# Kernel optimization log

Measured on AMD Instinct MI355X. Metric: run time of the kernel, lower is better.

Reference implementation:

```python
import jax, jax.numpy as jnp
import numpy as np

N_NODES = 100000
N_EDGES = 3200000
IN_DIM, HID1, HID2 = 128, 32, 16


def setup_inputs() -> dict:
    key = jax.random.key(0)
    ks = jax.random.split(key, 4)
    x = jax.random.normal(ks[0], (N_NODES, IN_DIM), dtype=jnp.float32)
    # glorot-ish scaling for weights
    W1 = jax.random.normal(ks[1], (IN_DIM, HID1), dtype=jnp.float32) * (1.0 / np.sqrt(IN_DIM))
    b1 = jnp.zeros((HID1,), dtype=jnp.float32)
    W2 = jax.random.normal(ks[2], (HID1, HID2), dtype=jnp.float32) * (1.0 / np.sqrt(HID1))
    b2 = jnp.zeros((HID2,), dtype=jnp.float32)
    edge_index = jax.random.randint(ks[3], (2, N_EDGES), 0, N_NODES, dtype=jnp.int64)
    return {"x": x, "W1": W1, "b1": b1, "W2": W2, "b2": b2, "edge_index": edge_index}


def _gcn_norm(edge_index, n_nodes):
    # add self loops, then symmetric normalization D^-1/2 (A+I) D^-1/2
    loops = jnp.arange(n_nodes, dtype=edge_index.dtype)
    src = jnp.concatenate([edge_index[0], loops])  # [E+N]
    dst = jnp.concatenate([edge_index[1], loops])
    deg = jax.ops.segment_sum(jnp.ones_like(dst, dtype=jnp.float32), dst, num_segments=n_nodes)
    inv_sqrt = jnp.where(deg > 0, jax.lax.rsqrt(jnp.maximum(deg, 1.0)), 0.0)
    norm = inv_sqrt[src] * inv_sqrt[dst]  # [E+N]
    return src, dst, norm


def _gcn_conv(x, W, b, src, dst, norm, n_nodes):
    xw = x @ W                                   # [N, out] transform first (out < in)
    msg = xw[src] * norm[:, None]                # gather + scale  [E+N, out]
    agg = jax.ops.segment_sum(msg, dst, num_segments=n_nodes)  # scatter-add
    return agg + b


def reference(x, W1, b1, W2, b2, edge_index):
    n = x.shape[0]
    src, dst, norm = _gcn_norm(edge_index, n)  # cached=True: same norm both layers
    h = _gcn_conv(x, W1, b1, src, dst, norm, n)
    h = jax.nn.relu(h)
    out = _gcn_conv(h, W2, b2, src, dst, norm, n)
    return out
```

## Files before the change

kernel.cpp:

```cpp
#include <hip/hip_runtime.h>
#include <hip/hip_fp16.h>


#define IN_DIM 128
#define HID1 32
#define HID2 16

#define BSHIFT 8
#define MAXNB 1024
#define SLABCAP 9216
#define P2_TILE 4096
#define P2_PER_THREAD 16

__device__ __forceinline__ void load_edge(const int* __restrict__ e32, int is64,
                                          long e, long E, int& s, int& d) {
    if (is64) { s = e32[2 * e];  d = e32[2 * E + 2 * e]; }
    else      { s = e32[e];      d = e32[E + e]; }
}

__device__ __forceinline__ void h8acc(float4& acc, uint2 u) {
    __half2 a = *(__half2*)&u.x, b = *(__half2*)&u.y;
    float2 fa = __half22float2(a), fb = __half22float2(b);
    acc.x += fa.x; acc.y += fa.y; acc.z += fb.x; acc.w += fb.y;
}

__global__ void init_cursors(const int* __restrict__ e32, int* __restrict__ flag,
                             int* __restrict__ total,
                             int* __restrict__ bucketCursor, int NB) {
    int i = blockIdx.x * blockDim.x + threadIdx.x;
    if (i < NB) bucketCursor[i] = i * SLABCAP;
    if (blockIdx.x == 0 && threadIdx.x == 0) {
        *total = 0;
        int is64 = 1;
        for (int k = 0; k < 64; ++k)
            if (e32[2 * k + 1] != 0) { is64 = 0; break; }
        *flag = is64;
    }
}

__global__ __launch_bounds__(256) void partition_edges(const int* __restrict__ e32,
                                                       const int* __restrict__ flag,
                                                       int* __restrict__ bucketCursor,
                                                       unsigned int* __restrict__ part,
                                                       int E, int NB) {
    __shared__ int lbase[MAXNB];
    for (int i = threadIdx.x; i < NB; i += 256) lbase[i] = 0;
    __syncthreads();
    int is64 = *flag;
    long e0 = (long)blockIdx.x * P2_TILE;
    unsigned int v[P2_PER_THREAD];
    int bb[P2_PER_THREAD];
#pragma unroll
    for (int i = 0; i < P2_PER_THREAD; ++i) {
        long e = e0 + threadIdx.x + i * 256;
        if (e < E) {
            int s, d;
            load_edge(e32, is64, e, E, s, d);
            bb[i] = d >> BSHIFT;
            v[i] = (unsigned int)s | ((unsigned int)(d & ((1 << BSHIFT) - 1)) << 17);
            atomicAdd(&lbase[bb[i]], 1);
        } else {
            bb[i] = -1;
        }
    }
    __syncthreads();
    for (int i = threadIdx.x; i < NB; i += 256) {
        int c = lbase[i];
        lbase[i] = c ? atomicAdd(&bucketCursor[i], c) : 0;
    }
    __syncthreads();
#pragma unroll
    for (int i = 0; i < P2_PER_THREAD; ++i) {
        if (bb[i] >= 0) {
            int pos = atomicAdd(&lbase[bb[i]], 1);
            if (pos < (bb[i] + 1) * SLABCAP)
                part[pos] = v[i];
        }
    }
}

__global__ __launch_bounds__(256) void build_rows(const unsigned int* __restrict__ part,
                                                  const int* __restrict__ bucketCursor,
                                                  int* __restrict__ total,
                                                  int* __restrict__ rowStart,
                                                  int* __restrict__ cnt,
                                                  float* __restrict__ inv,
                                                  int* __restrict__ srcs, int N) {
    __shared__ unsigned int sSlab[SLABCAP];
    __shared__ int lc[256];
    __shared__ int lofs[256];
    __shared__ int wsum[4];
    __shared__ int sGbase;
    int b = blockIdx.x;
    int sbeg = b * SLABCAP;
    int size = bucketCursor[b] - sbeg;
    if (size > SLABCAP) size = SLABCAP;
    int tid = threadIdx.x;
    lc[tid] = 0;
    __syncthreads();
    for (int i = tid; i < size; i += 256) {
        unsigned int v = part[sbeg + i];
        sSlab[i] = v;
        atomicAdd(&lc[v >> 17], 1);
    }
    if (tid == 0) sGbase = atomicAdd(total, size);
    __syncthreads();
    int gbase = sGbase;
    int c = lc[tid];
    int s = c;
#pragma unroll
    for (int off = 1; off < 64; off <<= 1) {
        int t = __shfl_up(s, off, 64);
        if ((tid & 63) >= off) s += t;
    }
    if ((tid & 63) == 63) wsum[tid >> 6] = s;
    __syncthreads();
    int wb = 0;
    for (int w = 0; w < (tid >> 6); ++w) wb += wsum[w];
    int gstart = gbase + wb + s - c;
    int n = (b << BSHIFT) + tid;
    if (n < N) {
        rowStart[n] = gstart;
        cnt[n] = c;
        inv[n] = rsqrtf((float)(c + 1));
    }
    lofs[tid] = gstart;
    __syncthreads();
    for (int i = tid; i < size; i += 256) {
        unsigned int v = sSlab[i];
        int pos = atomicAdd(&lofs[v >> 17], 1);
        srcs[pos] = (int)(v & 0x1FFFF);
    }
}

__global__ __launch_bounds__(256) void gemm1(const float* __restrict__ x,
                                             const float* __restrict__ W1,
                                             const float* __restrict__ inv,
                                             __half* __restrict__ xwh, int N) {
    __shared__ float4 sW4[IN_DIM * 8];
    for (int i = threadIdx.x; i < IN_DIM * 8; i += 256)
        sW4[i] = ((const float4*)W1)[i];
    __syncthreads();

    int rq = threadIdx.x >> 3;
    int cq = threadIdx.x & 7;
    int r0 = blockIdx.x * 128 + rq * 4;
    const float4* x4 = (const float4*)x;
    const float4 z4 = make_float4(0.f, 0.f, 0.f, 0.f);

    float4 acc[4];
#pragma unroll
    for (int i = 0; i < 4; ++i) acc[i] = z4;

    for (int k4 = 0; k4 < IN_DIM / 4; ++k4) {
        float4 xa[4];
#pragma unroll
        for (int i = 0; i < 4; ++i) {
            int r = r0 + i;
            xa[i] = (r < N) ? x4[(size_t)r * 32 + k4] : z4;
        }
#pragma unroll
        for (int kk = 0; kk < 4; ++kk) {
            float4 w = sW4[(k4 * 4 + kk) * 8 + cq];
#pragma unroll
            for (int i = 0; i < 4; ++i) {
                float xs = (kk == 0) ? xa[i].x : (kk == 1) ? xa[i].y
                         : (kk == 2) ? xa[i].z : xa[i].w;
                acc[i].x += xs * w.x;
                acc[i].y += xs * w.y;
                acc[i].z += xs * w.z;
                acc[i].w += xs * w.w;
            }
        }
    }

#pragma unroll
    for (int i = 0; i < 4; ++i) {
        int r = r0 + i;
        if (r <= N) {
            float sc = (r < N) ? inv[r] : 0.f;
            __half2 p0 = __floats2half2_rn(acc[i].x * sc, acc[i].y * sc);
            __half2 p1 = __floats2half2_rn(acc[i].z * sc, acc[i].w * sc);
            uint2 u;
            u.x = *(unsigned int*)&p0;
            u.y = *(unsigned int*)&p1;
            ((uint2*)xwh)[(size_t)r * 8 + cq] = u;
        }
    }
}

__global__ __launch_bounds__(256) void agg1_k(const int* __restrict__ rowStart,
                                              const int* __restrict__ cnt,
                                              const int* __restrict__ srcs,
                                              const float* __restrict__ inv,
                                              const __half* __restrict__ xwh,
                                              const float* __restrict__ b1,
                                              const float* __restrict__ W2,
                                              __half* __restrict__ hwh, int N) {
    __shared__ float sW2[HID1 * HID2];
    __shared__ float sAgg[4][HID1];
    for (int i = threadIdx.x; i < HID1 * HID2; i += 256) sW2[i] = W2[i];

    int w    = threadIdx.x >> 6;
    int lane = threadIdx.x & 63;
    int node = blockIdx.x * 4 + w;
    int nr   = (node < N) ? node : 0;
    int start = rowStart[nr];
    int len   = (node < N) ? cnt[nr] : 0;
    float invn = (node < N) ? inv[nr] : 0.f;
    int eg = lane >> 3;
    int r  = lane & 7;
    const uint2* xw2 = (const uint2*)xwh;

    int sv = (lane < len) ? srcs[start + lane] : N;
    uint2 selfv = xw2[(size_t)nr * 8 + r];

    uint2 vals[8];
#pragma unroll
    for (int g = 0; g < 8; ++g) {
        int jb = g * 8;
        if (jb < len) {
            int s = __shfl(sv, jb + eg, 64);
            vals[g] = xw2[(size_t)s * 8 + r];
        }
    }
    float4 acc = make_float4(0.f, 0.f, 0.f, 0.f);
    if (eg == 0) h8acc(acc, selfv);
#pragma unroll
    for (int g = 0; g < 8; ++g)
        if (g * 8 < len) h8acc(acc, vals[g]);

    for (int j = 64 + eg; j < len; j += 8)
        h8acc(acc, xw2[(size_t)srcs[start + j] * 8 + r]);

#pragma unroll
    for (int off = 32; off >= 8; off >>= 1) {
        acc.x += __shfl_down(acc.x, off, 64);
        acc.y += __shfl_down(acc.y, off, 64);
        acc.z += __shfl_down(acc.z, off, 64);
        acc.w += __shfl_down(acc.w, off, 64);
    }
    if (lane < 8) {
        float4 bb = ((const float4*)b1)[lane];
        float4 o;
        o.x = fmaxf(bb.x + invn * acc.x, 0.f);
        o.y = fmaxf(bb.y + invn * acc.y, 0.f);
        o.z = fmaxf(bb.z + invn * acc.z, 0.f);
        o.w = fmaxf(bb.w + invn * acc.w, 0.f);
        ((float4*)&sAgg[w][0])[lane] = o;
    }
    __syncthreads();

    if (lane < HID2 && node <= N) {
        float y = 0.f;
#pragma unroll
        for (int cc = 0; cc < HID1; ++cc)
            y += sAgg[w][cc] * sW2[cc * HID2 + lane];
        hwh[(size_t)node * HID2 + lane] = __float2half_rn(y * invn);
    }
}

__global__ __launch_bounds__(256) void agg2_k(const int* __restrict__ rowStart,
                                              const int* __restrict__ cnt,
                                              const int* __restrict__ srcs,
                                              const float* __restrict__ inv,
                                              const __half* __restrict__ hwh,
                                              const float* __restrict__ b2,
                                              float* __restrict__ out, int N) {
    int wave = (blockIdx.x * blockDim.x + threadIdx.x) >> 6;
    int lane = threadIdx.x & 63;
    if (wave >= N) return;
    int n = wave;
    int eg = lane >> 2;
    int q  = lane & 3;
    int start = rowStart[n];
    int len   = cnt[n];
    float invn = inv[n];
    const uint2* hw2 = (const uint2*)hwh;

    int sv = (lane < len) ? srcs[start + lane] : N;
    uint2 selfv = hw2[(size_t)n * 4 + q];

    uint2 vals[4];
#pragma unroll
    for (int g = 0; g < 4; ++g) {
        int jb = g * 16;
        if (jb < len) {
            int s = __shfl(sv, jb + eg, 64);
            vals[g] = hw2[(size_t)s * 4 + q];
        }
    }
    float4 acc = make_float4(0.f, 0.f, 0.f, 0.f);
    if (eg == 0) h8acc(acc, selfv);
#pragma unroll
    for (int g = 0; g < 4; ++g)
        if (g * 16 < len) h8acc(acc, vals[g]);

    for (int j = 64 + eg; j < len; j += 16)
        h8acc(acc, hw2[(size_t)srcs[start + j] * 4 + q]);

#pragma unroll
    for (int off = 32; off >= 4; off >>= 1) {
        acc.x += __shfl_down(acc.x, off, 64);
        acc.y += __shfl_down(acc.y, off, 64);
        acc.z += __shfl_down(acc.z, off, 64);
        acc.w += __shfl_down(acc.w, off, 64);
    }
    if (lane < 4) {
        float4 bb = ((const float4*)b2)[lane];
        float4 o;
        o.x = bb.x + invn * acc.x;
        o.y = bb.y + invn * acc.y;
        o.z = bb.z + invn * acc.z;
        o.w = bb.w + invn * acc.w;
        ((float4*)out)[(size_t)n * 4 + lane] = o;
    }
}

extern "C" void kernel_launch(void* const* d_in, const int* in_sizes, int n_in,
                              void* d_out, int out_size, void* d_ws, size_t ws_size,
                              hipStream_t stream) {
    const float* x  = (const float*)d_in[0];
    const float* W1 = (const float*)d_in[1];
    const float* b1 = (const float*)d_in[2];
    const float* W2 = (const float*)d_in[3];
    const float* b2 = (const float*)d_in[4];
    const int*  e32 = (const int*)d_in[5];
    float* out = (float*)d_out;

    const int N = in_sizes[0] / IN_DIM;
    const int E = in_sizes[5] / 2;
    const int Npad = ((N + 63) / 64) * 64;
    const int Epad = ((E + 63) / 64) * 64;
    const int NB   = (N + (1 << BSHIFT) - 1) >> BSHIFT;

    char* ws = (char*)d_ws;
    int*   flag         = (int*)ws;
    int*   total        = (int*)(ws + 64);
    int*   bucketCursor = (int*)(ws + 256);
    int*   cnt      = bucketCursor + 1088;
    int*   rowStart = cnt + Npad;
    float* inv      = (float*)(rowStart + Npad);
    int*   srcs     = (int*)(inv + Npad);
    size_t slabBytes = (size_t)NB * SLABCAP * 4;
    unsigned int* part = (unsigned int*)(srcs + Epad);
    __half* xwh = (__half*)part;
    __half* hwh = (__half*)((char*)part + slabBytes);

    init_cursors<<<(NB + 255) / 256, 256, 0, stream>>>(e32, flag, total,
                                                       bucketCursor, NB);
    partition_edges<<<(E + P2_TILE - 1) / P2_TILE, 256, 0, stream>>>(
        e32, flag, bucketCursor, part, E, NB);
    build_rows<<<NB, 256, 0, stream>>>(part, bucketCursor, total,
                                       rowStart, cnt, inv, srcs, N);

    gemm1<<<(N + 1 + 127) / 128, 256, 0, stream>>>(x, W1, inv, xwh, N);
    agg1_k<<<(N + 1 + 3) / 4, 256, 0, stream>>>(rowStart, cnt, srcs, inv, xwh,
                                                b1, W2, hwh, N);
    agg2_k<<<(N + 3) / 4, 256, 0, stream>>>(rowStart, cnt, srcs, inv, hwh,
                                            b2, out, N);
}
```

Measured before the change: 289.3 us.

## Split layer-1 feature table into two column halves aggregated in separate passes

```diff
diff --git a/kernel.cpp b/kernel.cpp
--- a/kernel.cpp
+++ b/kernel.cpp
@@ -136,7 +136,8 @@
 __global__ __launch_bounds__(256) void gemm1(const float* __restrict__ x,
                                              const float* __restrict__ W1,
                                              const float* __restrict__ inv,
-                                             __half* __restrict__ xwh, int N) {
+                                             __half* __restrict__ xwh0,
+                                             __half* __restrict__ xwh1, int N) {
     __shared__ float4 sW4[IN_DIM * 8];
     for (int i = threadIdx.x; i < IN_DIM * 8; i += 256)
         sW4[i] = ((const float4*)W1)[i];
@@ -174,6 +175,8 @@
         }
     }
 
+    __half* tab = (cq < 4) ? xwh0 : xwh1;
+    int cqi = cq & 3;
 #pragma unroll
     for (int i = 0; i < 4; ++i) {
         int r = r0 + i;
@@ -184,19 +187,68 @@
             uint2 u;
             u.x = *(unsigned int*)&p0;
             u.y = *(unsigned int*)&p1;
-            ((uint2*)xwh)[(size_t)r * 8 + cq] = u;
-        }
-    }
-}
-
-__global__ __launch_bounds__(256) void agg1_k(const int* __restrict__ rowStart,
-                                              const int* __restrict__ cnt,
-                                              const int* __restrict__ srcs,
-                                              const float* __restrict__ inv,
-                                              const __half* __restrict__ xwh,
-                                              const float* __restrict__ b1,
-                                              const float* __restrict__ W2,
-                                              __half* __restrict__ hwh, int N) {
+            ((uint2*)tab)[(size_t)r * 4 + cqi] = u;
+        }
+    }
+}
+
+__global__ __launch_bounds__(256) void agg1a_k(const int* __restrict__ rowStart,
+                                               const int* __restrict__ cnt,
+                                               const int* __restrict__ srcs,
+                                               const __half* __restrict__ xwh0,
+                                               float* __restrict__ partial, int N) {
+    int wave = (blockIdx.x * blockDim.x + threadIdx.x) >> 6;
+    int lane = threadIdx.x & 63;
+    int node = wave;
+    if (node > N) return;
+    int nr   = (node < N) ? node : 0;
+    int start = rowStart[nr];
+    int len   = (node < N) ? cnt[nr] : 0;
+    int eg = lane >> 2;
+    int q  = lane & 3;
+    const uint2* t0 = (const uint2*)xwh0;
+
+    int sv = (lane < len) ? srcs[start + lane] : N;
+    uint2 selfv = t0[(size_t)nr * 4 + q];
+
+    uint2 vals[4];
+#pragma unroll
+    for (int g = 0; g < 4; ++g) {
+        int jb = g * 16;
+        if (jb < len) {
+            int s = __shfl(sv, jb + eg, 64);
+            vals[g] = t0[(size_t)s * 4 + q];
+        }
+    }
+    float4 acc = make_float4(0.f, 0.f, 0.f, 0.f);
+    if (eg == 0) h8acc(acc, selfv);
+#pragma unroll
+    for (int g = 0; g < 4; ++g)
+        if (g * 16 < len) h8acc(acc, vals[g]);
+
+    for (int j = 64 + eg; j < len; j += 16)
+        h8acc(acc, t0[(size_t)srcs[start + j] * 4 + q]);
+
+#pragma unroll
+    for (int off = 32; off >= 4; off >>= 1) {
+        acc.x += __shfl_down(acc.x, off, 64);
+        acc.y += __shfl_down(acc.y, off, 64);
+        acc.z += __shfl_down(acc.z, off, 64);
+        acc.w += __shfl_down(acc.w, off, 64);
+    }
+    if (lane < 4)
+        ((float4*)partial)[(size_t)node * 4 + lane] = acc;
+}
+
+__global__ __launch_bounds__(256) void agg1b_k(const int* __restrict__ rowStart,
+                                               const int* __restrict__ cnt,
+                                               const int* __restrict__ srcs,
+                                               const float* __restrict__ inv,
+                                               const __half* __restrict__ xwh1,
+                                               const float* __restrict__ partial,
+                                               const float* __restrict__ b1,
+                                               const float* __restrict__ W2,
+                                               __half* __restrict__ hwh, int N) {
     __shared__ float sW2[HID1 * HID2];
     __shared__ float sAgg[4][HID1];
     for (int i = threadIdx.x; i < HID1 * HID2; i += 256) sW2[i] = W2[i];
@@ -208,50 +260,59 @@
     int start = rowStart[nr];
     int len   = (node < N) ? cnt[nr] : 0;
     float invn = (node < N) ? inv[nr] : 0.f;
-    int eg = lane >> 3;
-    int r  = lane & 7;
-    const uint2* xw2 = (const uint2*)xwh;
-
-    int sv = (lane < len) ? srcs[start + lane] : N;
-    uint2 selfv = xw2[(size_t)nr * 8 + r];
-
-    uint2 vals[8];
-#pragma unroll
-    for (int g = 0; g < 8; ++g) {
-        int jb = g * 8;
+    int eg = lane >> 2;
+    int q  = lane & 3;
+    const uint2* t1 = (const uint2*)xwh1;
+    bool live = (node <= N);
+
+    int sv = (live && lane < len) ? srcs[start + lane] : N;
+    uint2 selfv = t1[(size_t)nr * 4 + q];
+
+    uint2 vals[4];
+#pragma unroll
+    for (int g = 0; g < 4; ++g) {
+        int jb = g * 16;
         if (jb < len) {
             int s = __shfl(sv, jb + eg, 64);
-            vals[g] = xw2[(size_t)s * 8 + r];
+            vals[g] = t1[(size_t)s * 4 + q];
         }
     }
     float4 acc = make_float4(0.f, 0.f, 0.f, 0.f);
     if (eg == 0) h8acc(acc, selfv);
 #pragma unroll
-    for (int g = 0; g < 8; ++g)
-        if (g * 8 < len) h8acc(acc, vals[g]);
-
-    for (int j = 64 + eg; j < len; j += 8)
-        h8acc(acc, xw2[(size_t)srcs[start + j] * 8 + r]);
-
-#pragma unroll
-    for (int off = 32; off >= 8; off >>= 1) {
+    for (int g = 0; g < 4; ++g)
+        if (g * 16 < len) h8acc(acc, vals[g]);
+
+    for (int j = 64 + eg; j < len; j += 16)
+        h8acc(acc, t1[(size_t)srcs[start + j] * 4 + q]);
+
+#pragma unroll
+    for (int off = 32; off >= 4; off >>= 1) {
         acc.x += __shfl_down(acc.x, off, 64);
         acc.y += __shfl_down(acc.y, off, 64);
         acc.z += __shfl_down(acc.z, off, 64);
         acc.w += __shfl_down(acc.w, off, 64);
     }
-    if (lane < 8) {
-        float4 bb = ((const float4*)b1)[lane];
+    if (lane < 4 && live) {
+        float4 bh = ((const float4*)b1)[4 + lane];
         float4 o;
-        o.x = fmaxf(bb.x + invn * acc.x, 0.f);
-        o.y = fmaxf(bb.y + invn * acc.y, 0.f);
-        o.z = fmaxf(bb.z + invn * acc.z, 0.f);
-        o.w = fmaxf(bb.w + invn * acc.w, 0.f);
-        ((float4*)&sAgg[w][0])[lane] = o;
-    }
-    __syncthreads();
-
-    if (lane < HID2 && node <= N) {
+        o.x = fmaxf(bh.x + invn * acc.x, 0.f);
+        o.y = fmaxf(bh.y + invn * acc.y, 0.f);
+        o.z = fmaxf(bh.z + invn * acc.z, 0.f);
+        o.w = fmaxf(bh.w + invn * acc.w, 0.f);
+        ((float4*)&sAgg[w][16])[lane] = o;
+        float4 p = ((const float4*)partial)[(size_t)node * 4 + lane];
+        float4 bl = ((const float4*)b1)[lane];
+        float4 o0;
+        o0.x = fmaxf(bl.x + invn * p.x, 0.f);
+        o0.y = fmaxf(bl.y + invn * p.y, 0.f);
+        o0.z = fmaxf(bl.z + invn * p.z, 0.f);
+        o0.w = fmaxf(bl.w + invn * p.w, 0.f);
+        ((float4*)&sAgg[w][0])[lane] = o0;
+    }
+    __syncthreads();
+
+    if (lane < HID2 && live) {
         float y = 0.f;
 #pragma unroll
         for (int cc = 0; cc < HID1; ++cc)
@@ -343,9 +404,12 @@
     float* inv      = (float*)(rowStart + Npad);
     int*   srcs     = (int*)(inv + Npad);
     size_t slabBytes = (size_t)NB * SLABCAP * 4;
+    size_t halfTab   = (size_t)(N + 1) * 16 * sizeof(__half);
     unsigned int* part = (unsigned int*)(srcs + Epad);
-    __half* xwh = (__half*)part;
-    __half* hwh = (__half*)((char*)part + slabBytes);
+    __half* xwh0    = (__half*)part;
+    __half* xwh1    = (__half*)((char*)part + halfTab);
+    float*  partial = (float*)((char*)part + 2 * halfTab);
+    __half* hwh     = (__half*)((char*)part + slabBytes);
 
     init_cursors<<<(NB + 255) / 256, 256, 0, stream>>>(e32, flag, total,
                                                        bucketCursor, NB);
@@ -354,9 +418,11 @@
     build_rows<<<NB, 256, 0, stream>>>(part, bucketCursor, total,
                                        rowStart, cnt, inv, srcs, N);
 
-    gemm1<<<(N + 1 + 127) / 128, 256, 0, stream>>>(x, W1, inv, xwh, N);
-    agg1_k<<<(N + 1 + 3) / 4, 256, 0, stream>>>(rowStart, cnt, srcs, inv, xwh,
-                                                b1, W2, hwh, N);
+    gemm1<<<(N + 1 + 127) / 128, 256, 0, stream>>>(x, W1, inv, xwh0, xwh1, N);
+    agg1a_k<<<(N + 1 + 3) / 4, 256, 0, stream>>>(rowStart, cnt, srcs, xwh0,
+                                                 partial, N);
+    agg1b_k<<<(N + 1 + 3) / 4, 256, 0, stream>>>(rowStart, cnt, srcs, inv, xwh1,
+                                                 partial, b1, W2, hwh, N);
     agg2_k<<<(N + 3) / 4, 256, 0, stream>>>(rowStart, cnt, srcs, inv, hwh,
                                             b2, out, N);
 }
```

New measurement: 318.9 us. 1.1x slower.

## Halve destination buckets and restructure edge partitioning into larger two-pass tiles

Applied to the files above, without the earlier changes.

```diff
diff --git a/kernel.cpp b/kernel.cpp
--- a/kernel.cpp
+++ b/kernel.cpp
@@ -6,11 +6,10 @@
 #define HID1 32
 #define HID2 16
 
-#define BSHIFT 8
+#define BSHIFT 7
 #define MAXNB 1024
-#define SLABCAP 9216
-#define P2_TILE 4096
-#define P2_PER_THREAD 16
+#define SLABCAP 4736
+#define P2T 16384
 
 __device__ __forceinline__ void load_edge(const int* __restrict__ e32, int is64,
                                           long e, long E, int& s, int& d) {
@@ -38,44 +37,35 @@
     }
 }
 
-__global__ __launch_bounds__(256) void partition_edges(const int* __restrict__ e32,
-                                                       const int* __restrict__ flag,
-                                                       int* __restrict__ bucketCursor,
-                                                       unsigned int* __restrict__ part,
-                                                       int E, int NB) {
+__global__ __launch_bounds__(1024) void partition_edges(const int* __restrict__ e32,
+                                                        const int* __restrict__ flag,
+                                                        int* __restrict__ bucketCursor,
+                                                        unsigned int* __restrict__ part,
+                                                        int E, int NB) {
     __shared__ int lbase[MAXNB];
-    for (int i = threadIdx.x; i < NB; i += 256) lbase[i] = 0;
+    for (int i = threadIdx.x; i < NB; i += 1024) lbase[i] = 0;
     __syncthreads();
     int is64 = *flag;
-    long e0 = (long)blockIdx.x * P2_TILE;
-    unsigned int v[P2_PER_THREAD];
-    int bb[P2_PER_THREAD];
-#pragma unroll
-    for (int i = 0; i < P2_PER_THREAD; ++i) {
-        long e = e0 + threadIdx.x + i * 256;
-        if (e < E) {
-            int s, d;
-            load_edge(e32, is64, e, E, s, d);
-            bb[i] = d >> BSHIFT;
-            v[i] = (unsigned int)s | ((unsigned int)(d & ((1 << BSHIFT) - 1)) << 17);
-            atomicAdd(&lbase[bb[i]], 1);
-        } else {
-            bb[i] = -1;
-        }
-    }
-    __syncthreads();
-    for (int i = threadIdx.x; i < NB; i += 256) {
-        int c = lbase[i];
-        lbase[i] = c ? atomicAdd(&bucketCursor[i], c) : 0;
-    }
-    __syncthreads();
-#pragma unroll
-    for (int i = 0; i < P2_PER_THREAD; ++i) {
-        if (bb[i] >= 0) {
-            int pos = atomicAdd(&lbase[bb[i]], 1);
-            if (pos < (bb[i] + 1) * SLABCAP)
-                part[pos] = v[i];
-        }
+    long e0 = (long)blockIdx.x * P2T;
+    long eend = e0 + P2T; if (eend > E) eend = E;
+    for (long e = e0 + threadIdx.x; e < eend; e += 1024) {
+        int d = is64 ? e32[2 * E + 2 * e] : e32[E + e];
+        atomicAdd(&lbase[d >> BSHIFT], 1);
+    }
+    __syncthreads();
+    for (int b = threadIdx.x; b < NB; b += 1024) {
+        int c = lbase[b];
+        lbase[b] = c ? atomicAdd(&bucketCursor[b], c) : 0;
+    }
+    __syncthreads();
+    for (long e = e0 + threadIdx.x; e < eend; e += 1024) {
+        int s, d;
+        load_edge(e32, is64, e, E, s, d);
+        int bkt = d >> BSHIFT;
+        int pos = atomicAdd(&lbase[bkt], 1);
+        if (pos < (bkt + 1) * SLABCAP)
+            part[pos] = (unsigned int)s |
+                        ((unsigned int)(d & ((1 << BSHIFT) - 1)) << 17);
     }
 }
 
@@ -87,16 +77,16 @@
                                                   float* __restrict__ inv,
                                                   int* __restrict__ srcs, int N) {
     __shared__ unsigned int sSlab[SLABCAP];
-    __shared__ int lc[256];
-    __shared__ int lofs[256];
-    __shared__ int wsum[4];
+    __shared__ int lc[128];
+    __shared__ int lofs[128];
+    __shared__ int wsum[2];
     __shared__ int sGbase;
     int b = blockIdx.x;
     int sbeg = b * SLABCAP;
     int size = bucketCursor[b] - sbeg;
     if (size > SLABCAP) size = SLABCAP;
     int tid = threadIdx.x;
-    lc[tid] = 0;
+    if (tid < 128) lc[tid] = 0;
     __syncthreads();
     for (int i = tid; i < size; i += 256) {
         unsigned int v = part[sbeg + i];
@@ -105,26 +95,29 @@
     }
     if (tid == 0) sGbase = atomicAdd(total, size);
     __syncthreads();
-    int gbase = sGbase;
-    int c = lc[tid];
-    int s = c;
-#pragma unroll
-    for (int off = 1; off < 64; off <<= 1) {
-        int t = __shfl_up(s, off, 64);
-        if ((tid & 63) >= off) s += t;
-    }
-    if ((tid & 63) == 63) wsum[tid >> 6] = s;
-    __syncthreads();
-    int wb = 0;
-    for (int w = 0; w < (tid >> 6); ++w) wb += wsum[w];
-    int gstart = gbase + wb + s - c;
-    int n = (b << BSHIFT) + tid;
-    if (n < N) {
-        rowStart[n] = gstart;
-        cnt[n] = c;
-        inv[n] = rsqrtf((float)(c + 1));
-    }
-    lofs[tid] = gstart;
+    if (tid < 128) {
+        int gbase = sGbase;
+        int c = lc[tid];
+        int s = c;
+#pragma unroll
+        for (int off = 1; off < 64; off <<= 1) {
+            int t = __shfl_up(s, off, 64);
+            if ((tid & 63) >= off) s += t;
+        }
+        if ((tid & 63) == 63) wsum[tid >> 6] = s;
+        __syncthreads();
+        int wb = (tid >= 64) ? wsum[0] : 0;
+        int gstart = gbase + wb + s - c;
+        int n = (b << BSHIFT) + tid;
+        if (n < N) {
+            rowStart[n] = gstart;
+            cnt[n] = c;
+            inv[n] = rsqrtf((float)(c + 1));
+        }
+        lofs[tid] = gstart;
+    } else {
+        __syncthreads();
+    }
     __syncthreads();
     for (int i = tid; i < size; i += 256) {
         unsigned int v = sSlab[i];
@@ -349,7 +342,7 @@
 
     init_cursors<<<(NB + 255) / 256, 256, 0, stream>>>(e32, flag, total,
                                                        bucketCursor, NB);
-    partition_edges<<<(E + P2_TILE - 1) / P2_TILE, 256, 0, stream>>>(
+    partition_edges<<<(E + P2T - 1) / P2T, 1024, 0, stream>>>(
         e32, flag, bucketCursor, part, E, NB);
     build_rows<<<NB, 256, 0, stream>>>(part, bucketCursor, total,
                                        rowStart, cnt, inv, srcs, N);
```

Result: faster. 282.5 us (-2.4%).
